# Kernel optimization log

Hardware: AMD Instinct MI355X
Metric: run time of the kernel (lower is better)

The kernel has to match this reference:

```python
import jax, jax.numpy as jnp
import numpy as np

DN = ('NCHW', 'OIHW', 'NCHW')


def conv2d(x, w, b):
    y = jax.lax.conv_general_dilated(x, w, (1, 1), 'SAME', dimension_numbers=DN)
    return y + b[None, :, None, None]


def dyn_filter(x, Wa, ba, Wb, bb, Wc, bc):
    # KPN-style head: predict 81 per-pixel 9x9 filter taps, softmax-normalized.
    h = jax.nn.relu(conv2d(x, Wa, ba))
    h = jax.nn.relu(conv2d(h, Wb, bb))
    f = conv2d(h, Wc, bc)            # (N, 81, H, W)
    return jax.nn.softmax(f, axis=1)


def apply_dynamic_conv(x, f):
    # Equivalent to pad(4) + unfold(9x9) + mul + sum, without materializing
    # the (N,81,H,W)*... patch tensor: accumulate 81 shifted slices.
    N, C, H, W = x.shape  # C == 1
    xp = jnp.pad(x, ((0, 0), (0, 0), (4, 4), (4, 4)))
    out = jnp.zeros((N, 1, H, W), x.dtype)
    for dy in range(9):
        for dx in range(9):
            k = dy * 9 + dx  # matches unfold(2).unfold(3).permute(0,1,4,5,2,3) tap order
            out = out + xp[:, :, dy:dy + H, dx:dx + W] * f[:, k:k + 1]
    return out


def nearest_resize(x, oh, ow):
    _, _, ih, iw = x.shape
    ri = jnp.arange(oh) * ih // oh   # matches torch F.interpolate mode='nearest'
    rj = jnp.arange(ow) * iw // ow
    return x[:, :, ri][:, :, :, rj]


def setup_inputs() -> dict:
    key = jax.random.key(0)
    ks = jax.random.split(key, 8)
    s = 0.05
    return {
        'x': jax.random.normal(ks[0], (2, 1, 512, 512), jnp.float32),
        'g': jax.random.normal(ks[1], (2, 1, 512, 512), jnp.float32),
        'fWa': jax.random.normal(ks[2], (5, 64, 1, 3, 3), jnp.float32) * s,
        'fba': jnp.zeros((5, 64), jnp.float32),
        'fWb': jax.random.normal(ks[3], (5, 64, 64, 3, 3), jnp.float32) * s,
        'fbb': jnp.zeros((5, 64), jnp.float32),
        'fWc': jax.random.normal(ks[4], (5, 81, 64, 3, 3), jnp.float32) * s,
        'fbc': jnp.zeros((5, 81), jnp.float32),
        'W2a': jax.random.normal(ks[5], (64, 5, 3, 3), jnp.float32) * s,
        'b2a': jnp.zeros((64,), jnp.float32),
        'W2b': jax.random.normal(ks[6], (1, 64, 3, 3), jnp.float32) * s,
        'b2b': jnp.zeros((1,), jnp.float32),
    }


def reference(x, g, fWa, fba, fWb, fbb, fWc, fbc, W2a, b2a, W2b, b2b):
    N, C, h, w = x.shape
    scales = [
        x,
        nearest_resize(x, h // 2, w // 2),
        nearest_resize(x, h // 4, w // 4),
        nearest_resize(x, h // 8, w // 8),
        g,
    ]
    outs = []
    for i, s in enumerate(scales):
        f = dyn_filter(s, fWa[i], fba[i], fWb[i], fbb[i], fWc[i], fbc[i])
        y = apply_dynamic_conv(s, f)
        if y.shape[2] != h or y.shape[3] != w:
            y = nearest_resize(y, h, w)
        outs.append(y)
    cat = jnp.concatenate(outs, axis=1)  # (N, 5, h, w)
    hid = jax.nn.relu(conv2d(cat, W2a, b2a))
    return conv2d(hid, W2b, b2b)
```

## Files before the change

### kernel.cpp

```cpp
#include <hip/hip_runtime.h>
#include <math.h>

typedef _Float16 half8 __attribute__((ext_vector_type(8)));
typedef _Float16 half4v __attribute__((ext_vector_type(4)));
typedef float f32x4 __attribute__((ext_vector_type(4)));

#define LOG2E 1.44269504f

__device__ __forceinline__ void pack_generic(int rem, int NT, int COUT, float scale,
                                             const float* __restrict__ src,
                                             _Float16* __restrict__ dst) {
  int j = rem & 7, lane = (rem >> 3) & 63, rest = rem >> 9;
  int t = rest % NT, s = rest / NT;
  int oc = t * 16 + (lane & 15);
  int tap = s >> 1;
  int ic = (s & 1) * 32 + ((lane >> 4) & 3) * 8 + j;
  float v = (oc < COUT) ? src[((size_t)oc * 64 + ic) * 9 + tap] * scale : 0.f;
  dst[rem] = (_Float16)v;
}

__global__ void pack_all_kernel(const float* __restrict__ fWa, const float* __restrict__ fWb,
                                const float* __restrict__ fWc, const float* __restrict__ W2a,
                                const float* __restrict__ W2b,
                                _Float16* __restrict__ Bp1, _Float16* __restrict__ BpA,
                                _Float16* __restrict__ BpB, _Float16* __restrict__ Bpb,
                                _Float16* __restrict__ Bpc) {
  int idx = blockIdx.x * blockDim.x + threadIdx.x;
  if (idx < 184320) {
    int sc = idx / 36864, rem = idx - sc * 36864;
    pack_generic(rem, 4, 64, 1.f, fWb + sc * 36864, Bpb + sc * 36864);
  } else if (idx < 460800) {
    int i2 = idx - 184320;
    int sc = i2 / 55296, rem = i2 - sc * 55296;
    pack_generic(rem, 6, 81, LOG2E, fWc + sc * 46656, Bpc + sc * 55296);
  } else if (idx < 471040) {
    int i2 = idx - 460800;
    int sc = i2 >> 11, rem = i2 & 2047;
    int j = rem & 7, lane = (rem >> 3) & 63, nt = rem >> 9;
    int oc = nt * 16 + (lane & 15);
    int k = ((lane >> 4) & 3) * 8 + j;
    float v = (k < 9) ? fWa[sc * 576 + oc * 9 + k] : 0.f;
    Bp1[sc * 2048 + rem] = (_Float16)v;
  } else if (idx < 475136) {
    int rem = idx - 471040;
    int j = rem & 7, lane = (rem >> 3) & 63;
    int nt = (rem >> 9) & 3, s = rem >> 11;
    int oc = nt * 16 + (lane & 15);
    int k = s * 32 + ((lane >> 4) & 3) * 8 + j;
    float v = 0.f;
    if (k < 45) { int ic = k / 9, tap = k - ic * 9; v = W2a[(oc * 5 + ic) * 9 + tap]; }
    BpA[rem] = (_Float16)v;
  } else if (idx < 484352) {
    pack_generic(idx - 475136, 1, 1, 1.f, W2b, BpB);
  }
}

__global__ void down_all_kernel(const float* __restrict__ x, _Float16* __restrict__ s1,
                                _Float16* __restrict__ s2, _Float16* __restrict__ s3) {
  int idx = blockIdx.x * blockDim.x + threadIdx.x;
  if (idx < 131072) {
    int n = idx >> 16, p = idx & 65535, rr = p >> 8, cc = p & 255;
    s1[idx] = (_Float16)x[(size_t)n * 262144 + (size_t)(rr * 2) * 512 + cc * 2];
  } else if (idx < 163840) {
    int i2 = idx - 131072;
    int n = i2 >> 14, p = i2 & 16383, rr = p >> 7, cc = p & 127;
    s2[i2] = (_Float16)x[(size_t)n * 262144 + (size_t)(rr * 4) * 512 + cc * 4];
  } else if (idx < 172032) {
    int i2 = idx - 163840;
    int n = i2 >> 12, p = i2 & 4095, rr = p >> 6, cc = p & 63;
    s3[i2] = (_Float16)x[(size_t)n * 262144 + (size_t)(rr * 8) * 512 + cc * 8];
  }
}

__device__ __forceinline__ void map_block(int bid, int& sc, int& n, int& bx, int& by,
                                          int& Hs, int& RS, int& h2off) {
  if (bid < 2048) { sc = 0; Hs = 512; RS = 1; h2off = 0;
    int t = bid; n = t >> 10; t &= 1023; by = t >> 5; bx = t & 31; }
  else if (bid < 4096) { sc = 4; Hs = 512; RS = 1; h2off = 33554432;
    int t = bid - 2048; n = t >> 10; t &= 1023; by = t >> 5; bx = t & 31; }
  else if (bid < 4608) { sc = 1; Hs = 256; RS = 2; h2off = 67108864;
    int t = bid - 4096; n = t >> 8; t &= 255; by = t >> 4; bx = t & 15; }
  else if (bid < 4736) { sc = 2; Hs = 128; RS = 4; h2off = 75497472;
    int t = bid - 4608; n = t >> 6; t &= 63; by = t >> 3; bx = t & 7; }
  else { sc = 3; Hs = 64; RS = 8; h2off = 77594624;
    int t = bid - 4736; n = t >> 4; t &= 15; by = t >> 2; bx = t & 3; }
}

__device__ __forceinline__ const void* pick_src(int sc, const float* x, const float* g,
                                                const _Float16* s1, const _Float16* s2,
                                                const _Float16* s3, int& sStr, bool& f16s) {
  if (sc == 0) { sStr = 262144; f16s = false; return x; }
  if (sc == 1) { sStr = 65536; f16s = true; return s1; }
  if (sc == 2) { sStr = 16384; f16s = true; return s2; }
  if (sc == 3) { sStr = 4096; f16s = true; return s3; }
  sStr = 262144; f16s = false; return g;
}

__device__ __forceinline__ float src_load(const void* p, bool f16s, size_t off) {
  return f16s ? (float)((const _Float16*)p)[off] : ((const float*)p)[off];
}

template <int NT, bool SWAP>
__device__ __forceinline__ void mfma_acc18(const _Float16* slab, const half8* __restrict__ Bp,
                                           f32x4 (&acc)[4][NT], int tid) {
  const int lane = tid & 63;
  const int wv = tid >> 6;
  const int quad = lane >> 4;
  const int ln15 = lane & 15;
  const f32x4 zz = {0.f, 0.f, 0.f, 0.f};
#pragma unroll
  for (int mt = 0; mt < 4; ++mt)
#pragma unroll
    for (int nt = 0; nt < NT; ++nt) acc[mt][nt] = zz;
#pragma unroll 1
  for (int s = 0; s < 18; ++s) {
    const int tap = s >> 1;
    const int dy = tap / 3;
    const int dx = tap - dy * 3;
    half8 bf[NT];
#pragma unroll
    for (int nt = 0; nt < NT; ++nt) bf[nt] = Bp[(s * NT + nt) * 64 + lane];
    const int C = dx + ln15;
    const int qsw = (((s & 1) * 4 + quad) ^ (C & 7));
    const _Float16* base = slab + C * 64 + qsw * 8;
    half8 af[4];
#pragma unroll
    for (int mt = 0; mt < 4; ++mt) {
      const int R = wv * 4 + mt + dy;
      af[mt] = *(const half8*)(base + R * (18 * 64));
    }
#pragma unroll
    for (int mt = 0; mt < 4; ++mt)
#pragma unroll
      for (int nt = 0; nt < NT; ++nt)
        acc[mt][nt] = SWAP
          ? __builtin_amdgcn_mfma_f32_16x16x32_f16(bf[nt], af[mt], acc[mt][nt], 0, 0, 0)
          : __builtin_amdgcn_mfma_f32_16x16x32_f16(af[mt], bf[nt], acc[mt][nt], 0, 0, 0);
  }
}

template <int NT, int COUT, int COUTP, bool RELU, typename OutT>
__device__ __forceinline__ void mfma_body(const _Float16* slab, const half8* __restrict__ Bp,
                                          const float* __restrict__ bias,
                                          OutT* __restrict__ out,
                                          int H, int W, int gr0, int gc0, int tid) {
  f32x4 acc[4][NT];
  mfma_acc18<NT, false>(slab, Bp, acc, tid);
  const int lane = tid & 63;
  const int wv = tid >> 6;
  const int quad = lane >> 4;
  const int ln15 = lane & 15;
  float bvv[NT];
#pragma unroll
  for (int nt = 0; nt < NT; ++nt) {
    const int oc = nt * 16 + ln15;
    bvv[nt] = (oc < COUT) ? bias[oc] : 0.f;
  }
#pragma unroll
  for (int mt = 0; mt < 4; ++mt) {
    const int gr = gr0 + wv * 4 + mt;
#pragma unroll
    for (int reg = 0; reg < 4; ++reg) {
      const int gc = gc0 + quad * 4 + reg;
#pragma unroll
      for (int nt = 0; nt < NT; ++nt) {
        const int oc = nt * 16 + ln15;
        float v = acc[mt][nt][reg] + bvv[nt];
        if (RELU) v = fmaxf(v, 0.f);
        if (oc < COUTP) out[((size_t)gr * W + gc) * COUTP + oc] = (OutT)v;
      }
    }
  }
}

__global__ __launch_bounds__(256)
void conv12_ms_kernel(const float* __restrict__ x, const float* __restrict__ g,
                      const _Float16* __restrict__ s1, const _Float16* __restrict__ s2,
                      const _Float16* __restrict__ s3,
                      const half8* __restrict__ Bp1b, const float* __restrict__ fba,
                      const half8* __restrict__ Bpbb, const float* __restrict__ fbb,
                      _Float16* __restrict__ h2) {
  __shared__ float xs[20 * 20];
  __shared__ __align__(16) _Float16 slab[18 * 18 * 64];
  int sc, n, bx, by, Hs, RS, h2off;
  map_block(blockIdx.x, sc, n, bx, by, Hs, RS, h2off);
  int sStr; bool f16s;
  const void* src = pick_src(sc, x, g, s1, s2, s3, sStr, f16s);
  _Float16* out = h2 + h2off + (size_t)n * Hs * Hs * 64;
  const half8* Bp1 = Bp1b + sc * 256;
  const half8* Bp = Bpbb + sc * 4608;
  const float* ba = fba + sc * 64;
  const float* bb = fbb + sc * 64;
  const int H = Hs, W = Hs;
  const int tid = threadIdx.x;
  const int gr0 = by * 16, gc0 = bx * 16;
  for (int i = tid; i < 400; i += 256) {
    int R = i / 20, C = i % 20;
    int gr = gr0 - 2 + R, gc = gc0 - 2 + C;
    xs[i] = (gr >= 0 && gr < H && gc >= 0 && gc < W)
                ? src_load(src, f16s, (size_t)n * sStr + (size_t)gr * W + gc) : 0.f;
  }
  __syncthreads();
  const int lane = tid & 63;
  const int wv = tid >> 6;
  const int quad = lane >> 4;
  const int ln15 = lane & 15;
  half8 bf1[4];
  float b1v[4][4];
#pragma unroll
  for (int nt = 0; nt < 4; ++nt) {
    bf1[nt] = Bp1[nt * 64 + lane];
#pragma unroll
    for (int reg = 0; reg < 4; ++reg) b1v[nt][reg] = ba[nt * 16 + quad * 4 + reg];
  }
  int off1[8];
  bool v1[8];
#pragma unroll
  for (int j = 0; j < 8; ++j) {
    int k = quad * 8 + j;
    v1[j] = (k < 9);
    off1[j] = v1[j] ? ((k / 3) * 20 + (k % 3)) : 0;
  }
  const f32x4 zz = {0.f, 0.f, 0.f, 0.f};
#pragma unroll 1
  for (int mt = wv; mt < 21; mt += 4) {
    int p = mt * 16 + ln15;
    int pcl = (p < 323) ? p : 323;
    int Rg = pcl / 18, Cg = pcl - Rg * 18;
    int base = Rg * 20 + Cg;
    half8 af;
#pragma unroll
    for (int j = 0; j < 8; ++j)
      af[j] = v1[j] ? (_Float16)xs[base + off1[j]] : (_Float16)0.f;
    f32x4 a1[4] = {zz, zz, zz, zz};
#pragma unroll
    for (int nt = 0; nt < 4; ++nt)
      a1[nt] = __builtin_amdgcn_mfma_f32_16x16x32_f16(bf1[nt], af, a1[nt], 0, 0, 0);
    if (p < 324) {
      int R2 = p / 18, C2 = p - R2 * 18;
      int gr = gr0 - 1 + R2, gc = gc0 - 1 + C2;
      bool inb = (gr >= 0 && gr < H && gc >= 0 && gc < W);
      _Float16* sb = slab + p * 64 + (quad & 1) * 4;
      const int csw = C2 & 7;
#pragma unroll
      for (int nt = 0; nt < 4; ++nt) {
        half4v w;
#pragma unroll
        for (int reg = 0; reg < 4; ++reg) {
          float v = inb ? fmaxf(a1[nt][reg] + b1v[nt][reg], 0.f) : 0.f;
          w[reg] = (_Float16)v;
        }
        const int chunk = nt * 2 + (quad >> 1);
        *(half4v*)(sb + ((chunk ^ csw) * 8)) = w;
      }
    }
  }
  __syncthreads();
  mfma_body<4, 64, 64, true, _Float16>(slab, Bp, bb, out, H, W, gr0, gc0, tid);
}

__global__ __launch_bounds__(256)
void conv3sd_ms_kernel(const _Float16* __restrict__ h2, const half8* __restrict__ Bpcb,
                       const float* __restrict__ fbc,
                       const float* __restrict__ x, const float* __restrict__ g,
                       const _Float16* __restrict__ s1, const _Float16* __restrict__ s2,
                       const _Float16* __restrict__ s3, float* __restrict__ cat) {
  __shared__ __align__(16) _Float16 slab[18 * 18 * 64];
  __shared__ float xs[24 * 24];
  int sc, n, bx, by, Hs, RS, h2off;
  map_block(blockIdx.x, sc, n, bx, by, Hs, RS, h2off);
  int sStr; bool f16s;
  const void* src = pick_src(sc, x, g, s1, s2, s3, sStr, f16s);
  const _Float16* in = h2 + h2off + (size_t)n * Hs * Hs * 64;
  const half8* Bp = Bpcb + sc * 6912;
  const float* bias = fbc + sc * 81;
  float* catn = cat + (size_t)n * 1310720;
  const int H = Hs, W = Hs;
  const int tid = threadIdx.x;
  const int gr0 = by * 16, gc0 = bx * 16;
  for (int i = tid; i < 18 * 18 * 8; i += 256) {
    int chunk = i & 7, px = i >> 3;
    int R = px / 18, C = px % 18;
    int gr = gr0 - 1 + R, gc = gc0 - 1 + C;
    half8 v = {0, 0, 0, 0, 0, 0, 0, 0};
    if (gr >= 0 && gr < H && gc >= 0 && gc < W)
      v = *(const half8*)(in + ((size_t)gr * W + gc) * 64 + chunk * 8);
    *(half8*)(slab + px * 64 + (chunk ^ (C & 7)) * 8) = v;
  }
  for (int i = tid; i < 576; i += 256) {
    int R = i / 24, C = i % 24;
    int gr = gr0 - 4 + R, gc = gc0 - 4 + C;
    xs[i] = (gr >= 0 && gr < H && gc >= 0 && gc < W)
                ? src_load(src, f16s, (size_t)n * sStr + (size_t)gr * W + gc) : 0.f;
  }
  __syncthreads();
  f32x4 acc[4][6];
  mfma_acc18<6, true>(slab, Bp, acc, tid);
  const int lane = tid & 63;
  const int wv = tid >> 6;
  const int quad = lane >> 4;
  const int ln15 = lane & 15;
  float bvv[6][4];
  int dyx[6][4];
  bool vv[6][4];
#pragma unroll
  for (int nt = 0; nt < 6; ++nt)
#pragma unroll
    for (int reg = 0; reg < 4; ++reg) {
      int ch = nt * 16 + quad * 4 + reg;
      bool ok = (ch < 81);
      vv[nt][reg] = ok;
      bvv[nt][reg] = ok ? bias[ch] * LOG2E : 0.f;
      int dy = ch / 9, dx = ch - dy * 9;
      dyx[nt][reg] = ok ? dy * 24 + dx : 0;
    }
  const int lrs = (RS == 2) ? 1 : ((RS == 4) ? 2 : 3);
#pragma unroll
  for (int mt = 0; mt < 4; ++mt) {
    const float* xb = xs + (wv * 4 + mt) * 24 + ln15;
    float sum = 0.f, y = 0.f;
#pragma unroll
    for (int nt = 0; nt < 6; ++nt)
#pragma unroll
      for (int reg = 0; reg < 4; ++reg) {
        if (vv[nt][reg]) {
          float e = exp2f(acc[mt][nt][reg] + bvv[nt][reg]);
          sum += e;
          y = fmaf(e, xb[dyx[nt][reg]], y);
        }
      }
    sum += __shfl_xor(sum, 16, 64);
    sum += __shfl_xor(sum, 32, 64);
    y += __shfl_xor(y, 16, 64);
    y += __shfl_xor(y, 32, 64);
    const float o = y / sum;
    const int gr = gr0 + wv * 4 + mt, gc = gc0 + ln15;
    if (RS == 1) {
      if (quad == 0) catn[((size_t)gr * 512 + gc) * 5 + sc] = o;
    } else {
      for (int t = quad; t < RS * RS; t += 4) {
        int a = t >> lrs, b = t & (RS - 1);
        catn[((size_t)(gr * RS + a) * 512 + (gc * RS + b)) * 5 + sc] = o;
      }
    }
  }
}

__global__ __launch_bounds__(256)
void tail_fused_kernel(const float* __restrict__ cat,
                       const half8* __restrict__ BpA, const float* __restrict__ b2a,
                       const half8* __restrict__ BpB, const float* __restrict__ b2b,
                       float* __restrict__ out) {
  __shared__ float cs[20 * 20 * 5];
  __shared__ __align__(16) _Float16 hid[18 * 18 * 64];
  const int n = blockIdx.z;
  const float* cin = cat + (size_t)n * (512 * 512 * 5);
  float* op = out + (size_t)n * (512 * 512);
  const int tid = threadIdx.x;
  const int gr0 = blockIdx.y * 16, gc0 = blockIdx.x * 16;
  for (int i = tid; i < 2000; i += 256) {
    int px = i / 5, ic = i - px * 5;
    int R = px / 20, C = px - R * 20;
    int gr = gr0 - 2 + R, gc = gc0 - 2 + C;
    cs[i] = (gr >= 0 && gr < 512 && gc >= 0 && gc < 512)
                ? cin[((size_t)gr * 512 + gc) * 5 + ic] : 0.f;
  }
  __syncthreads();
  const int lane = tid & 63;
  const int wv = tid >> 6;
  const int quad = lane >> 4;
  const int ln15 = lane & 15;
  int goff[2][8];
  bool gok[2][8];
#pragma unroll
  for (int s = 0; s < 2; ++s)
#pragma unroll
    for (int j = 0; j < 8; ++j) {
      int k = s * 32 + quad * 8 + j;
      bool ok = (k < 45);
      int ic = k / 9;
      int tap = k - ic * 9;
      int dy = tap / 3, dx = tap - dy * 3;
      goff[s][j] = ok ? ((dy * 20 + dx) * 5 + ic) : 0;
      gok[s][j] = ok;
    }
  half8 bfA[2][4];
  float bAv[4][4];
#pragma unroll
  for (int s = 0; s < 2; ++s)
#pragma unroll
    for (int nt = 0; nt < 4; ++nt) bfA[s][nt] = BpA[(s * 4 + nt) * 64 + lane];
#pragma unroll
  for (int nt = 0; nt < 4; ++nt)
#pragma unroll
    for (int reg = 0; reg < 4; ++reg) bAv[nt][reg] = b2a[nt * 16 + quad * 4 + reg];
  const f32x4 zz = {0.f, 0.f, 0.f, 0.f};
#pragma unroll 1
  for (int mt = wv; mt < 21; mt += 4) {
    int p = mt * 16 + ln15;
    int pcl = (p < 323) ? p : 323;
    int base = (pcl / 18) * 100 + (pcl % 18) * 5;
    f32x4 acc1[4] = {zz, zz, zz, zz};
#pragma unroll
    for (int s = 0; s < 2; ++s) {
      half8 af;
#pragma unroll
      for (int j = 0; j < 8; ++j) {
        float a = gok[s][j] ? cs[base + goff[s][j]] : 0.f;
        af[j] = (_Float16)a;
      }
#pragma unroll
      for (int nt = 0; nt < 4; ++nt)
        acc1[nt] = __builtin_amdgcn_mfma_f32_16x16x32_f16(bfA[s][nt], af, acc1[nt], 0, 0, 0);
    }
    if (p < 324) {
      int R2 = p / 18, C2 = p - R2 * 18;
      int gr = gr0 - 1 + R2, gc = gc0 - 1 + C2;
      bool inb = (gr >= 0 && gr < 512 && gc >= 0 && gc < 512);
      _Float16* sb = hid + p * 64 + (quad & 1) * 4;
      const int csw = C2 & 7;
#pragma unroll
      for (int nt = 0; nt < 4; ++nt) {
        half4v w;
#pragma unroll
        for (int reg = 0; reg < 4; ++reg) {
          float v = inb ? fmaxf(acc1[nt][reg] + bAv[nt][reg], 0.f) : 0.f;
          w[reg] = (_Float16)v;
        }
        const int chunk = nt * 2 + (quad >> 1);
        *(half4v*)(sb + ((chunk ^ csw) * 8)) = w;
      }
    }
  }
  __syncthreads();
  mfma_body<1, 1, 1, false, float>(hid, BpB, b2b, op, 512, 512, gr0, gc0, tid);
}

extern "C" void kernel_launch(void* const* d_in, const int* in_sizes, int n_in,
                              void* d_out, int out_size, void* d_ws, size_t ws_size,
                              hipStream_t stream) {
  (void)in_sizes; (void)n_in; (void)out_size; (void)ws_size;
  const float* x   = (const float*)d_in[0];
  const float* g   = (const float*)d_in[1];
  const float* fWa = (const float*)d_in[2];
  const float* fba = (const float*)d_in[3];
  const float* fWb = (const float*)d_in[4];
  const float* fbb = (const float*)d_in[5];
  const float* fWc = (const float*)d_in[6];
  const float* fbc = (const float*)d_in[7];
  const float* W2a = (const float*)d_in[8];
  const float* b2a = (const float*)d_in[9];
  const float* W2b = (const float*)d_in[10];
  const float* b2b = (const float*)d_in[11];
  float* out = (float*)d_out;
  float* ws = (float*)d_ws;

  float* Bp1F = ws;
  float* BpAF = Bp1F + 5120;
  float* BpBF = BpAF + 2048;
  float* BpbF = BpBF + 4608;
  float* BpcF = BpbF + 92160;
  float* s1F  = BpcF + 138240;
  float* s2F  = s1F + 65536;
  float* s3F  = s2F + 16384;
  float* cat  = s3F + 4096;
  float* h2F  = cat + 2621440;
  _Float16* s1 = (_Float16*)s1F;
  _Float16* s2 = (_Float16*)s2F;
  _Float16* s3 = (_Float16*)s3F;
  _Float16* h2 = (_Float16*)h2F;
  const half8* Bp1 = (const half8*)Bp1F;
  const half8* BpA = (const half8*)BpAF;
  const half8* BpB = (const half8*)BpBF;
  const half8* Bpb = (const half8*)BpbF;
  const half8* Bpc = (const half8*)BpcF;

  pack_all_kernel<<<1892, 256, 0, stream>>>(fWa, fWb, fWc, W2a, W2b,
                                            (_Float16*)Bp1F, (_Float16*)BpAF,
                                            (_Float16*)BpBF, (_Float16*)BpbF,
                                            (_Float16*)BpcF);
  down_all_kernel<<<672, 256, 0, stream>>>(x, s1, s2, s3);
  conv12_ms_kernel<<<4768, 256, 0, stream>>>(x, g, s1, s2, s3, Bp1, fba, Bpb, fbb, h2);
  conv3sd_ms_kernel<<<4768, 256, 0, stream>>>(h2, Bpc, fbc, x, g, s1, s2, s3, cat);
  tail_fused_kernel<<<dim3(32, 32, 2), 256, 0, stream>>>(cat, BpA, b2a, BpB, b2b, out);
}
```

Baseline: 454.2 us.

## Split final conv slab load into two channel halves; store cat planar

The per-scale final conv now stages its 18x18x64 fp16 input halo in two 32-channel halves in a smaller padded LDS slab (stride 40), with the MFMA loop inlined per half. This cuts LDS use, which may allow more resident blocks, at the cost of an extra barrier and reloading. The concatenated intermediate changes from pixel-interleaved (5 channels per pixel) to planar per scale and batch, so each store writes contiguous rows instead of stride-5 scattered floats. The tail kernel's gather is updated to match the new layout.

```diff
diff --git a/kernel.cpp b/kernel.cpp
--- a/kernel.cpp
+++ b/kernel.cpp
@@ -265,7 +265,7 @@
                        const float* __restrict__ x, const float* __restrict__ g,
                        const _Float16* __restrict__ s1, const _Float16* __restrict__ s2,
                        const _Float16* __restrict__ s3, float* __restrict__ cat) {
-  __shared__ __align__(16) _Float16 slab[18 * 18 * 64];
+  __shared__ __align__(16) _Float16 slab[324 * 40];
   __shared__ float xs[24 * 24];
   int sc, n, bx, by, Hs, RS, h2off;
   map_block(blockIdx.x, sc, n, bx, by, Hs, RS, h2off);
@@ -274,32 +274,61 @@
   const _Float16* in = h2 + h2off + (size_t)n * Hs * Hs * 64;
   const half8* Bp = Bpcb + sc * 6912;
   const float* bias = fbc + sc * 81;
-  float* catn = cat + (size_t)n * 1310720;
+  float* catp = cat + (size_t)(sc * 2 + n) * 262144;
   const int H = Hs, W = Hs;
   const int tid = threadIdx.x;
   const int gr0 = by * 16, gc0 = bx * 16;
-  for (int i = tid; i < 18 * 18 * 8; i += 256) {
-    int chunk = i & 7, px = i >> 3;
-    int R = px / 18, C = px % 18;
-    int gr = gr0 - 1 + R, gc = gc0 - 1 + C;
-    half8 v = {0, 0, 0, 0, 0, 0, 0, 0};
-    if (gr >= 0 && gr < H && gc >= 0 && gc < W)
-      v = *(const half8*)(in + ((size_t)gr * W + gc) * 64 + chunk * 8);
-    *(half8*)(slab + px * 64 + (chunk ^ (C & 7)) * 8) = v;
-  }
+  const int lane = tid & 63;
+  const int wv = tid >> 6;
+  const int quad = lane >> 4;
+  const int ln15 = lane & 15;
   for (int i = tid; i < 576; i += 256) {
     int R = i / 24, C = i % 24;
     int gr = gr0 - 4 + R, gc = gc0 - 4 + C;
     xs[i] = (gr >= 0 && gr < H && gc >= 0 && gc < W)
                 ? src_load(src, f16s, (size_t)n * sStr + (size_t)gr * W + gc) : 0.f;
   }
-  __syncthreads();
   f32x4 acc[4][6];
-  mfma_acc18<6, true>(slab, Bp, acc, tid);
-  const int lane = tid & 63;
-  const int wv = tid >> 6;
-  const int quad = lane >> 4;
-  const int ln15 = lane & 15;
+  const f32x4 zz = {0.f, 0.f, 0.f, 0.f};
+#pragma unroll
+  for (int mt = 0; mt < 4; ++mt)
+#pragma unroll
+    for (int nt = 0; nt < 6; ++nt) acc[mt][nt] = zz;
+#pragma unroll 1
+  for (int h = 0; h < 2; ++h) {
+    if (h) __syncthreads();
+    for (int i = tid; i < 1296; i += 256) {
+      int chunk = i & 3, px = i >> 2;
+      int R = px / 18, C = px - R * 18;
+      int gr = gr0 - 1 + R, gc = gc0 - 1 + C;
+      half8 v = {0, 0, 0, 0, 0, 0, 0, 0};
+      if (gr >= 0 && gr < H && gc >= 0 && gc < W)
+        v = *(const half8*)(in + ((size_t)gr * W + gc) * 64 + (h * 4 + chunk) * 8);
+      *(half8*)(slab + px * 40 + chunk * 8) = v;
+    }
+    __syncthreads();
+#pragma unroll 1
+    for (int tap = 0; tap < 9; ++tap) {
+      const int dy = tap / 3;
+      const int dx = tap - dy * 3;
+      half8 bf[6];
+#pragma unroll
+      for (int nt = 0; nt < 6; ++nt) bf[nt] = Bp[(((tap * 2 + h) * 6) + nt) * 64 + lane];
+      const int C = dx + ln15;
+      const _Float16* base = slab + C * 40 + quad * 8;
+      half8 af[4];
+#pragma unroll
+      for (int mt = 0; mt < 4; ++mt) {
+        const int R = wv * 4 + mt + dy;
+        af[mt] = *(const half8*)(base + R * 720);
+      }
+#pragma unroll
+      for (int mt = 0; mt < 4; ++mt)
+#pragma unroll
+        for (int nt = 0; nt < 6; ++nt)
+          acc[mt][nt] = __builtin_amdgcn_mfma_f32_16x16x32_f16(bf[nt], af[mt], acc[mt][nt], 0, 0, 0);
+    }
+  }
   float bvv[6][4];
   int dyx[6][4];
   bool vv[6][4];
@@ -336,11 +365,11 @@
     const float o = y / sum;
     const int gr = gr0 + wv * 4 + mt, gc = gc0 + ln15;
     if (RS == 1) {
-      if (quad == 0) catn[((size_t)gr * 512 + gc) * 5 + sc] = o;
+      if (quad == 0) catp[(size_t)gr * 512 + gc] = o;
     } else {
       for (int t = quad; t < RS * RS; t += 4) {
         int a = t >> lrs, b = t & (RS - 1);
-        catn[((size_t)(gr * RS + a) * 512 + (gc * RS + b)) * 5 + sc] = o;
+        catp[((size_t)(gr * RS + a)) * 512 + (gc * RS + b)] = o;
       }
     }
   }
@@ -354,16 +383,15 @@
   __shared__ float cs[20 * 20 * 5];
   __shared__ __align__(16) _Float16 hid[18 * 18 * 64];
   const int n = blockIdx.z;
-  const float* cin = cat + (size_t)n * (512 * 512 * 5);
   float* op = out + (size_t)n * (512 * 512);
   const int tid = threadIdx.x;
   const int gr0 = blockIdx.y * 16, gc0 = blockIdx.x * 16;
   for (int i = tid; i < 2000; i += 256) {
-    int px = i / 5, ic = i - px * 5;
+    int ic = i / 400, px = i - ic * 400;
     int R = px / 20, C = px - R * 20;
     int gr = gr0 - 2 + R, gc = gc0 - 2 + C;
-    cs[i] = (gr >= 0 && gr < 512 && gc >= 0 && gc < 512)
-                ? cin[((size_t)gr * 512 + gc) * 5 + ic] : 0.f;
+    cs[px * 5 + ic] = (gr >= 0 && gr < 512 && gc >= 0 && gc < 512)
+                ? cat[(size_t)(ic * 2 + n) * 262144 + (size_t)gr * 512 + gc] : 0.f;
   }
   __syncthreads();
   const int lane = tid & 63;
```

After: 414.4 us. -8.8%, faster.
